# Performance work log

Hardware: AMD Instinct MI355X
Metric: run time of the kernel (lower is better)

The kernel has to match this reference:

```python
import jax, jax.numpy as jnp
import numpy as np

N_NODES = 100000
N_EDGES = 1600000
C_IN = 63
C_OUT = 63


def _glorot(key, shape):
    lim = (6.0 / (shape[0] + shape[1])) ** 0.5
    return jax.random.uniform(key, shape, jnp.float32, -lim, lim)


def setup_inputs() -> dict:
    key = jax.random.key(0)
    ks = jax.random.split(key, 10)
    t = jax.random.uniform(ks[0], (1,), jnp.float32)
    data = jax.random.normal(ks[1], (N_NODES, C_IN), jnp.float32)
    edges = jax.random.randint(ks[2], (2, N_EDGES), 0, N_NODES, jnp.int64)
    pos = jax.random.normal(ks[3], (N_NODES, 3), jnp.float32)
    edge_attr = jax.random.uniform(ks[4], (N_EDGES,), jnp.float32)
    # GCNConv(c_in+1, 64) -> GCNConv(64, 32) -> GCNConv(32, c_out)
    W1 = _glorot(ks[5], (C_IN + 1, 64)); b1 = jnp.zeros((64,), jnp.float32)
    W2 = _glorot(ks[6], (64, 32));       b2 = jnp.zeros((32,), jnp.float32)
    W3 = _glorot(ks[7], (32, C_OUT));    b3 = jnp.zeros((C_OUT,), jnp.float32)
    return {"t": t, "data": data, "edges": edges, "pos": pos,
            "edge_attr": edge_attr, "W1": W1, "b1": b1, "W2": W2,
            "b2": b2, "W3": W3, "b3": b3}


def _gcn_conv(x, W, b, row, col, norm, self_norm, n):
    # PyG GCNConv: linear, then normalized scatter-add aggregation (+self-loop), then bias
    x = x @ W                                                    # [N, F_out]
    out = jax.ops.segment_sum(x[row] * norm[:, None], col, num_segments=n)
    out = out + x * self_norm[:, None]                           # self-loop term
    return out + b


def reference(t, data, edges, pos, edge_attr, W1, b1, W2, b2, W3, b3):
    n = data.shape[0]
    row, col = edges[0], edges[1]                                # source j, target i
    ew = edge_attr.astype(jnp.float32)
    # gcn_norm with self-loops (fill_value=1): deg over target incl. self-loop
    deg = jax.ops.segment_sum(ew, col, num_segments=n) + 1.0
    dis = jnp.where(deg > 0, jax.lax.rsqrt(deg), 0.0)
    norm = dis[row] * ew * dis[col]                              # [E]
    self_norm = dis * dis                                        # [N]
    # time channel concat
    tt = jnp.ones((n, 1), data.dtype) * t
    h = jnp.concatenate([tt, data.astype(jnp.float32)], axis=1)  # [N, c_in+1]
    h = jnp.tanh(_gcn_conv(h, W1, b1, row, col, norm, self_norm, n))
    h = jnp.tanh(_gcn_conv(h, W2, b2, row, col, norm, self_norm, n))
    return _gcn_conv(h, W3, b3, row, col, norm, self_norm, n)
```

## Files before the change

kernel.cpp:

```cpp
#include <hip/hip_runtime.h>
#include <hip/hip_fp16.h>


static inline int cdiv64(long long a, int b) { return (int)((a + b - 1) / b); }

#define BSH 8
#define BCAP 8192
#define CHUNK 4096

typedef _Float16 half8v __attribute__((ext_vector_type(8)));
union F4H8 { float4 f4; half8v h; };

__device__ __forceinline__ float tanh_fast(float x) {
  float t = __expf(2.0f * x);
  float r = __builtin_amdgcn_rcpf(t + 1.0f);
  return fmaf(-2.0f, r, 1.0f);
}

__global__ void zero_kernel(int4* __restrict__ p, int n4) {
  int i = blockIdx.x * blockDim.x + threadIdx.x;
  if (i < n4) p[i] = make_int4(0, 0, 0, 0);
}

__global__ __launch_bounds__(256) void bucket1_kernel(
    const int* __restrict__ row, const int* __restrict__ col,
    const float* __restrict__ ew, int* __restrict__ gcur,
    uint2* __restrict__ btmp, int nE, int nb) {
  __shared__ int hcnt[512];
  __shared__ int gbase[512];
  const int tid = threadIdx.x;
  const int e0 = blockIdx.x * CHUNK;
  const int cnt_e = min(CHUNK, nE - e0);
  for (int i = tid; i < nb; i += 256) hcnt[i] = 0;
  __syncthreads();

  uint2 recs[CHUNK / 256];
  int   bs[CHUNK / 256];
  int   lis[CHUNK / 256];
#pragma unroll
  for (int p = 0; p < CHUNK / 256; ++p) {
    int k = tid + p * 256;
    bool valid = k < cnt_e;
    int e = e0 + (valid ? k : 0);
    int c = col[e];
    unsigned q = __float2uint_rn(ew[e] * 32768.0f);
    if (q > 32767u) q = 32767u;
    uint2 r;
    r.x = (q << 17) | (unsigned)row[e];
    r.y = (unsigned)c;
    int b = c >> BSH;
    recs[p] = r;
    bs[p] = valid ? b : -1;
    lis[p] = valid ? atomicAdd(&hcnt[b], 1) : 0;
  }
  __syncthreads();
  for (int i = tid; i < nb; i += 256)
    gbase[i] = hcnt[i] ? atomicAdd(&gcur[i], hcnt[i]) : 0;
  __syncthreads();
#pragma unroll
  for (int p = 0; p < CHUNK / 256; ++p) {
    int b = bs[p];
    if (b >= 0) {
      int idx = gbase[b] + lis[p];
      if (idx < BCAP) btmp[((size_t)b << 13) + idx] = recs[p];
    }
  }
}

__global__ __launch_bounds__(256) void bucket2_kernel(
    const int* __restrict__ gcur, const uint2* __restrict__ btmp,
    uint2* __restrict__ ce, int2* __restrict__ node2,
    float* __restrict__ dis, int n) {
  __shared__ uint2 recs[BCAP];
  __shared__ uint2 stageA[BCAP / 2];
  __shared__ uint2 stageB[BCAP / 2];
  __shared__ unsigned cnt[256], sumq[256], start[256], cur[256], scanbuf[256];
  const int tid = threadIdx.x;
  const int b = blockIdx.x;
  const int cb = min(gcur[b], BCAP);
  const int colbase = b << BSH;
  const int ncols = min(256, n - colbase);

  cnt[tid] = 0; sumq[tid] = 0; cur[tid] = 0;
  const uint2* src = btmp + ((size_t)b << 13);
  for (int k = tid; k < cb; k += 256) recs[k] = src[k];
  __syncthreads();
  for (int k = tid; k < cb; k += 256) {
    unsigned cl = recs[k].y & 255u;
    atomicAdd(&cnt[cl], 1u);
    atomicAdd(&sumq[cl], recs[k].x >> 17);
  }
  __syncthreads();
  unsigned v = cnt[tid];
  unsigned incl = v;
  scanbuf[tid] = incl;
  __syncthreads();
  for (int off = 1; off < 256; off <<= 1) {
    unsigned add = (tid >= off) ? scanbuf[tid - off] : 0u;
    __syncthreads();
    incl += add;
    scanbuf[tid] = incl;
    __syncthreads();
  }
  start[tid] = incl - v;
  __syncthreads();
  for (int k = tid; k < cb; k += 256) {
    unsigned rw = recs[k].x;
    unsigned cl = recs[k].y & 255u;
    unsigned p = start[cl] + atomicAdd(&cur[cl], 1u);
    uint2 o;
    o.x = rw & 0x1FFFFu;
    o.y = __float_as_uint((float)(rw >> 17) * 3.0517578125e-05f);
    if (p < (unsigned)(BCAP / 2)) stageA[p] = o;
    else stageB[p - BCAP / 2] = o;
  }
  __syncthreads();
  const unsigned base = (unsigned)b << 13;
  for (int k = tid; k < cb; k += 256)
    ce[base + k] = (k < BCAP / 2) ? stageA[k] : stageB[k - BCAP / 2];
  if (tid < ncols) {
    node2[colbase + tid] = make_int2((int)(base + start[tid]), (int)cnt[tid]);
    float deg = (float)sumq[tid] * 3.0517578125e-05f + 1.0f;
    dis[colbase + tid] = rsqrtf(deg);
  }
}

__global__ __launch_bounds__(256) void gemm1_tiled(const float* __restrict__ data,
                                                   const float* __restrict__ tptr,
                                                   const float* __restrict__ W,
                                                   const float* __restrict__ dis,
                                                   __half2* __restrict__ y, int n) {
  __shared__ float Ws[64 * 64];
  __shared__ float Ds[64 * 63];
  const int tid = threadIdx.x;
  {
    const float4* W4 = (const float4*)W;
    float4* Ws4 = (float4*)Ws;
#pragma unroll
    for (int p = 0; p < 4; ++p) Ws4[p * 256 + tid] = W4[p * 256 + tid];
  }
  const float tv = tptr[0];
  const int rbase = blockIdx.x * 64;
  const int limit = min(64, n - rbase) * 63;
  {
    const float4* s4 = (const float4*)(data + (size_t)rbase * 63);
    float4* d4 = (float4*)Ds;
    const int n4 = limit >> 2;
#pragma unroll
    for (int p = 0; p < 4; ++p) {
      int idx = p * 256 + tid;
      if (idx < n4) d4[idx] = s4[idx];
    }
    int tail = limit & 3;
    if (tid < tail) Ds[(n4 << 2) + tid] = data[(size_t)rbase * 63 + (n4 << 2) + tid];
  }
  __syncthreads();
  const int tx = tid & 15, ty = tid >> 4;
  const float* a0p = &Ds[(4 * ty + 0) * 63];
  const float* a1p = &Ds[(4 * ty + 1) * 63];
  const float* a2p = &Ds[(4 * ty + 2) * 63];
  const float* a3p = &Ds[(4 * ty + 3) * 63];
  float acc[4][4];
  {
    float4 w0 = *(const float4*)&Ws[4 * tx];
#pragma unroll
    for (int i = 0; i < 4; ++i) {
      acc[i][0] = tv * w0.x; acc[i][1] = tv * w0.y;
      acc[i][2] = tv * w0.z; acc[i][3] = tv * w0.w;
    }
  }
#pragma unroll 3
  for (int k = 0; k < 63; ++k) {
    float4 w4 = *(const float4*)&Ws[(k + 1) * 64 + 4 * tx];
    float a0 = a0p[k], a1 = a1p[k], a2 = a2p[k], a3 = a3p[k];
    acc[0][0] = fmaf(a0, w4.x, acc[0][0]); acc[0][1] = fmaf(a0, w4.y, acc[0][1]);
    acc[0][2] = fmaf(a0, w4.z, acc[0][2]); acc[0][3] = fmaf(a0, w4.w, acc[0][3]);
    acc[1][0] = fmaf(a1, w4.x, acc[1][0]); acc[1][1] = fmaf(a1, w4.y, acc[1][1]);
    acc[1][2] = fmaf(a1, w4.z, acc[1][2]); acc[1][3] = fmaf(a1, w4.w, acc[1][3]);
    acc[2][0] = fmaf(a2, w4.x, acc[2][0]); acc[2][1] = fmaf(a2, w4.y, acc[2][1]);
    acc[2][2] = fmaf(a2, w4.z, acc[2][2]); acc[2][3] = fmaf(a2, w4.w, acc[2][3]);
    acc[3][0] = fmaf(a3, w4.x, acc[3][0]); acc[3][1] = fmaf(a3, w4.y, acc[3][1]);
    acc[3][2] = fmaf(a3, w4.z, acc[3][2]); acc[3][3] = fmaf(a3, w4.w, acc[3][3]);
  }
#pragma unroll
  for (int i = 0; i < 4; ++i) {
    int r = rbase + 4 * ty + i;
    if (r < n) {
      float di = dis[r];
      __half2* yp = y + (long long)r * 32 + 2 * tx;
      yp[0] = __floats2half2_rn(acc[i][0] * di, acc[i][1] * di);
      yp[1] = __floats2half2_rn(acc[i][2] * di, acc[i][3] * di);
    }
  }
}

__global__ void gather64h(const __half2* __restrict__ x, const uint2* __restrict__ ce,
                          const int2* __restrict__ node2, const float* __restrict__ dis,
                          const float* __restrict__ b, __half2* __restrict__ o, int n) {
  int i = blockIdx.x * 4 + (threadIdx.x >> 6);
  if (i >= n) return;
  int lane = threadIdx.x & 63;
  int g = lane >> 3;
  int f8 = lane & 7;
  int2 sc = node2[i];
  const uint2* cb = ce + sc.x;
  int c = sc.y;
  const float4* xf = (const float4*)x;
  float4 accA = {0.f, 0.f, 0.f, 0.f}, accB = {0.f, 0.f, 0.f, 0.f};
  int k = g;
  uint2 rec = (k < c) ? cb[k] : make_uint2(0u, 0u);
  while (k < c) {
    int kn = k + 8;
    uint2 recn = (kn < c) ? cb[kn] : make_uint2(0u, 0u);
    float w = __uint_as_float(rec.y);
    F4H8 u; u.f4 = xf[(size_t)rec.x * 8 + f8];
    accA.x = fmaf((float)u.h[0], w, accA.x);
    accA.y = fmaf((float)u.h[1], w, accA.y);
    accA.z = fmaf((float)u.h[2], w, accA.z);
    accA.w = fmaf((float)u.h[3], w, accA.w);
    accB.x = fmaf((float)u.h[4], w, accB.x);
    accB.y = fmaf((float)u.h[5], w, accB.y);
    accB.z = fmaf((float)u.h[6], w, accB.z);
    accB.w = fmaf((float)u.h[7], w, accB.w);
    rec = recn; k = kn;
  }
#pragma unroll
  for (int d = 8; d <= 32; d <<= 1) {
    accA.x += __shfl_xor(accA.x, d, 64); accA.y += __shfl_xor(accA.y, d, 64);
    accA.z += __shfl_xor(accA.z, d, 64); accA.w += __shfl_xor(accA.w, d, 64);
    accB.x += __shfl_xor(accB.x, d, 64); accB.y += __shfl_xor(accB.y, d, 64);
    accB.z += __shfl_xor(accB.z, d, 64); accB.w += __shfl_xor(accB.w, d, 64);
  }
  if (g == 0) {
    F4H8 s; s.f4 = xf[(size_t)i * 8 + f8];
    float di = dis[i];
    float4 b0 = ((const float4*)b)[2 * f8];
    float4 b1 = ((const float4*)b)[2 * f8 + 1];
    float v0 = tanh_fast(di * (accA.x + (float)s.h[0]) + b0.x);
    float v1 = tanh_fast(di * (accA.y + (float)s.h[1]) + b0.y);
    float v2 = tanh_fast(di * (accA.z + (float)s.h[2]) + b0.z);
    float v3 = tanh_fast(di * (accA.w + (float)s.h[3]) + b0.w);
    float v4 = tanh_fast(di * (accB.x + (float)s.h[4]) + b1.x);
    float v5 = tanh_fast(di * (accB.y + (float)s.h[5]) + b1.y);
    float v6 = tanh_fast(di * (accB.z + (float)s.h[6]) + b1.z);
    float v7 = tanh_fast(di * (accB.w + (float)s.h[7]) + b1.w);
    __half2 r0 = __floats2half2_rn(v0, v1);
    __half2 r1 = __floats2half2_rn(v2, v3);
    __half2 r2 = __floats2half2_rn(v4, v5);
    __half2 r3 = __floats2half2_rn(v6, v7);
    float4 st;
    st.x = *reinterpret_cast<float*>(&r0);
    st.y = *reinterpret_cast<float*>(&r1);
    st.z = *reinterpret_cast<float*>(&r2);
    st.w = *reinterpret_cast<float*>(&r3);
    ((float4*)o)[(size_t)i * 8 + f8] = st;
  }
}

template <bool TANH, bool BIAS, bool POSTDIS, bool FOUT>
__global__ void gather32h(const __half2* __restrict__ x, const uint2* __restrict__ ce,
                          const int2* __restrict__ node2, const float* __restrict__ dis,
                          const float* __restrict__ b, void* __restrict__ outv, int n) {
  int i = blockIdx.x * 4 + (threadIdx.x >> 6);
  if (i >= n) return;
  int lane = threadIdx.x & 63;
  int g = lane >> 2;
  int f8 = lane & 3;
  int2 sc = node2[i];
  const uint2* cb = ce + sc.x;
  int c = sc.y;
  const float4* xf = (const float4*)x;
  float4 accA = {0.f, 0.f, 0.f, 0.f}, accB = {0.f, 0.f, 0.f, 0.f};
  int k = g;
  uint2 rec = (k < c) ? cb[k] : make_uint2(0u, 0u);
  while (k < c) {
    int kn = k + 16;
    uint2 recn = (kn < c) ? cb[kn] : make_uint2(0u, 0u);
    float w = __uint_as_float(rec.y);
    F4H8 u; u.f4 = xf[(size_t)rec.x * 4 + f8];
    accA.x = fmaf((float)u.h[0], w, accA.x);
    accA.y = fmaf((float)u.h[1], w, accA.y);
    accA.z = fmaf((float)u.h[2], w, accA.z);
    accA.w = fmaf((float)u.h[3], w, accA.w);
    accB.x = fmaf((float)u.h[4], w, accB.x);
    accB.y = fmaf((float)u.h[5], w, accB.y);
    accB.z = fmaf((float)u.h[6], w, accB.z);
    accB.w = fmaf((float)u.h[7], w, accB.w);
    rec = recn; k = kn;
  }
#pragma unroll
  for (int d = 4; d <= 32; d <<= 1) {
    accA.x += __shfl_xor(accA.x, d, 64); accA.y += __shfl_xor(accA.y, d, 64);
    accA.z += __shfl_xor(accA.z, d, 64); accA.w += __shfl_xor(accA.w, d, 64);
    accB.x += __shfl_xor(accB.x, d, 64); accB.y += __shfl_xor(accB.y, d, 64);
    accB.z += __shfl_xor(accB.z, d, 64); accB.w += __shfl_xor(accB.w, d, 64);
  }
  if (g == 0) {
    F4H8 s; s.f4 = xf[(size_t)i * 4 + f8];
    float di = dis[i];
    float v0 = di * (accA.x + (float)s.h[0]);
    float v1 = di * (accA.y + (float)s.h[1]);
    float v2 = di * (accA.z + (float)s.h[2]);
    float v3 = di * (accA.w + (float)s.h[3]);
    float v4 = di * (accB.x + (float)s.h[4]);
    float v5 = di * (accB.y + (float)s.h[5]);
    float v6 = di * (accB.z + (float)s.h[6]);
    float v7 = di * (accB.w + (float)s.h[7]);
    if (BIAS) {
      float4 b0 = ((const float4*)b)[2 * f8];
      float4 b1 = ((const float4*)b)[2 * f8 + 1];
      v0 += b0.x; v1 += b0.y; v2 += b0.z; v3 += b0.w;
      v4 += b1.x; v5 += b1.y; v6 += b1.z; v7 += b1.w;
    }
    if (TANH) {
      v0 = tanh_fast(v0); v1 = tanh_fast(v1); v2 = tanh_fast(v2); v3 = tanh_fast(v3);
      v4 = tanh_fast(v4); v5 = tanh_fast(v5); v6 = tanh_fast(v6); v7 = tanh_fast(v7);
    }
    if (POSTDIS) {
      v0 *= di; v1 *= di; v2 *= di; v3 *= di;
      v4 *= di; v5 *= di; v6 *= di; v7 *= di;
    }
    if (FOUT) {
      ((float4*)outv)[(size_t)i * 8 + 2 * f8]     = make_float4(v0, v1, v2, v3);
      ((float4*)outv)[(size_t)i * 8 + 2 * f8 + 1] = make_float4(v4, v5, v6, v7);
    } else {
      __half2 r0 = __floats2half2_rn(v0, v1);
      __half2 r1 = __floats2half2_rn(v2, v3);
      __half2 r2 = __floats2half2_rn(v4, v5);
      __half2 r3 = __floats2half2_rn(v6, v7);
      float4 st;
      st.x = *reinterpret_cast<float*>(&r0);
      st.y = *reinterpret_cast<float*>(&r1);
      st.z = *reinterpret_cast<float*>(&r2);
      st.w = *reinterpret_cast<float*>(&r3);
      ((float4*)outv)[(size_t)i * 4 + f8] = st;
    }
  }
}

__global__ __launch_bounds__(256) void gemm2t(const __half2* __restrict__ h1,
                                              const float* __restrict__ W,
                                              const float* __restrict__ dis,
                                              __half2* __restrict__ y2, int n) {
  __shared__ float As[64 * 65];
  __shared__ float Ws[64 * 32];
  const int tid = threadIdx.x;
  const int rbase = blockIdx.x * 64;
  const int rows = min(64, n - rbase);
  {
    const float4* W4 = (const float4*)W;
    float4* Ws4 = (float4*)Ws;
    Ws4[tid] = W4[tid];
    Ws4[256 + tid] = W4[256 + tid];
  }
  {
    const __half2* src = h1 + (size_t)rbase * 32;
    const int limit = rows * 32;
#pragma unroll
    for (int p = 0; p < 8; ++p) {
      int idx = p * 256 + tid;
      if (idx < limit) {
        float2 f = __half22float2(src[idx]);
        int r = idx >> 5, k2 = idx & 31;
        As[r * 65 + 2 * k2] = f.x;
        As[r * 65 + 2 * k2 + 1] = f.y;
      }
    }
  }
  __syncthreads();
  const int tx = tid & 7, ty = tid >> 3;
  const float* a0p = &As[(2 * ty) * 65];
  const float* a1p = &As[(2 * ty + 1) * 65];
  float acc0[4] = {0.f, 0.f, 0.f, 0.f};
  float acc1[4] = {0.f, 0.f, 0.f, 0.f};
#pragma unroll 4
  for (int k = 0; k < 64; ++k) {
    float4 w4 = *(const float4*)&Ws[k * 32 + 4 * tx];
    float a0 = a0p[k], a1 = a1p[k];
    acc0[0] = fmaf(a0, w4.x, acc0[0]); acc0[1] = fmaf(a0, w4.y, acc0[1]);
    acc0[2] = fmaf(a0, w4.z, acc0[2]); acc0[3] = fmaf(a0, w4.w, acc0[3]);
    acc1[0] = fmaf(a1, w4.x, acc1[0]); acc1[1] = fmaf(a1, w4.y, acc1[1]);
    acc1[2] = fmaf(a1, w4.z, acc1[2]); acc1[3] = fmaf(a1, w4.w, acc1[3]);
  }
  int r0 = rbase + 2 * ty, r1 = r0 + 1;
  if (r0 < n) {
    float di = dis[r0];
    __half2 h0 = __floats2half2_rn(acc0[0] * di, acc0[1] * di);
    __half2 h1v = __floats2half2_rn(acc0[2] * di, acc0[3] * di);
    float2 st;
    st.x = *reinterpret_cast<float*>(&h0);
    st.y = *reinterpret_cast<float*>(&h1v);
    ((float2*)y2)[(size_t)r0 * 8 + tx] = st;
  }
  if (r1 < n) {
    float di = dis[r1];
    __half2 h0 = __floats2half2_rn(acc1[0] * di, acc1[1] * di);
    __half2 h1v = __floats2half2_rn(acc1[2] * di, acc1[3] * di);
    float2 st;
    st.x = *reinterpret_cast<float*>(&h0);
    st.y = *reinterpret_cast<float*>(&h1v);
    ((float2*)y2)[(size_t)r1 * 8 + tx] = st;
  }
}

__global__ __launch_bounds__(256) void gemm3_tiled(const float* __restrict__ agg,
                                                   const float* __restrict__ W,
                                                   const float* __restrict__ b,
                                                   float* __restrict__ out, int n) {
  __shared__ float As[64 * 33];
  __shared__ float Ws[32 * 64];
  const int tid = threadIdx.x;
  const int rbase = blockIdx.x * 64;
  const int rows = min(64, n - rbase);
  {
    int r = tid >> 6, j = tid & 63;
#pragma unroll
    for (int p = 0; p < 8; ++p) {
      int rr = r + p * 4;
      if (j < 63) Ws[rr * 64 + j] = W[rr * 63 + j];
    }
    const float* src = agg + (size_t)rbase * 32;
    const int limit = rows * 32;
#pragma unroll
    for (int p = 0; p < 8; ++p) {
      int idx = p * 256 + tid;
      if (idx < limit) As[(idx >> 5) * 33 + (idx & 31)] = src[idx];
    }
  }
  __syncthreads();
  const int tx = tid & 15, ty = tid >> 4;
  const float* a0p = &As[(4 * ty + 0) * 33];
  const float* a1p = &As[(4 * ty + 1) * 33];
  const float* a2p = &As[(4 * ty + 2) * 33];
  const float* a3p = &As[(4 * ty + 3) * 33];
  float bb[4];
#pragma unroll
  for (int jj = 0; jj < 4; ++jj) {
    int j = 4 * tx + jj;
    bb[jj] = (j < 63) ? b[j] : 0.f;
  }
  float acc[4][4];
#pragma unroll
  for (int i = 0; i < 4; ++i) {
    acc[i][0] = bb[0]; acc[i][1] = bb[1]; acc[i][2] = bb[2]; acc[i][3] = bb[3];
  }
#pragma unroll
  for (int k = 0; k < 32; ++k) {
    float4 w4 = *(const float4*)&Ws[k * 64 + 4 * tx];
    float a0 = a0p[k], a1 = a1p[k], a2 = a2p[k], a3 = a3p[k];
    acc[0][0] = fmaf(a0, w4.x, acc[0][0]); acc[0][1] = fmaf(a0, w4.y, acc[0][1]);
    acc[0][2] = fmaf(a0, w4.z, acc[0][2]); acc[0][3] = fmaf(a0, w4.w, acc[0][3]);
    acc[1][0] = fmaf(a1, w4.x, acc[1][0]); acc[1][1] = fmaf(a1, w4.y, acc[1][1]);
    acc[1][2] = fmaf(a1, w4.z, acc[1][2]); acc[1][3] = fmaf(a1, w4.w, acc[1][3]);
    acc[2][0] = fmaf(a2, w4.x, acc[2][0]); acc[2][1] = fmaf(a2, w4.y, acc[2][1]);
    acc[2][2] = fmaf(a2, w4.z, acc[2][2]); acc[2][3] = fmaf(a2, w4.w, acc[2][3]);
    acc[3][0] = fmaf(a3, w4.x, acc[3][0]); acc[3][1] = fmaf(a3, w4.y, acc[3][1]);
    acc[3][2] = fmaf(a3, w4.z, acc[3][2]); acc[3][3] = fmaf(a3, w4.w, acc[3][3]);
  }
#pragma unroll
  for (int i = 0; i < 4; ++i) {
    int r = rbase + 4 * ty + i;
    if (r < n) {
      float* op = out + (size_t)r * 63 + 4 * tx;
#pragma unroll
      for (int jj = 0; jj < 4; ++jj)
        if (4 * tx + jj < 63) op[jj] = acc[i][jj];
    }
  }
}

extern "C" void kernel_launch(void* const* d_in, const int* in_sizes, int n_in,
                              void* d_out, int out_size, void* d_ws, size_t ws_size,
                              hipStream_t stream) {
  const float* t    = (const float*)d_in[0];
  const float* data = (const float*)d_in[1];
  const int*   edges = (const int*)d_in[2];
  const float* ew = (const float*)d_in[4];
  const float* W1 = (const float*)d_in[5];
  const float* b1 = (const float*)d_in[6];
  const float* W2 = (const float*)d_in[7];
  const float* b2 = (const float*)d_in[8];
  const float* W3 = (const float*)d_in[9];
  const float* b3 = (const float*)d_in[10];
  float* out = (float*)d_out;

  const int n  = in_sizes[1] / 63;
  const int nE = in_sizes[4];
  const int* row = edges;
  const int* col = edges + nE;
  const int nb = (n + 255) >> 8;

  float* ws    = (float*)d_ws;
  float* dis   = ws;
  int2*  node2 = (int2*)(ws + n);
  int*   gcur  = (int*)(ws + 3 * (size_t)n);
  uint2* ce    = (uint2*)(ws + 3 * (size_t)n + 512);
  size_t ceW   = (size_t)nb * BCAP;
  float* regA  = (float*)(ce + ceW);
  float* regB  = regA + (size_t)n * 32;
  uint2* btmp  = (uint2*)regA;

  const int B = 256;

  zero_kernel<<<1, 128, 0, stream>>>((int4*)gcur, 128);
  bucket1_kernel<<<cdiv64(nE, CHUNK), 256, 0, stream>>>(row, col, ew, gcur, btmp, nE, nb);
  bucket2_kernel<<<nb, 256, 0, stream>>>(gcur, btmp, ce, node2, dis, n);

  gemm1_tiled<<<cdiv64(n, 64), 256, 0, stream>>>(data, t, W1, dis, (__half2*)regA, n);
  gather64h<<<cdiv64(n, 4), B, 0, stream>>>((const __half2*)regA, ce, node2, dis, b1,
                                            (__half2*)regB, n);
  gemm2t<<<cdiv64(n, 64), 256, 0, stream>>>((const __half2*)regB, W2, dis, (__half2*)regA, n);
  gather32h<true, true, true, false><<<cdiv64(n, 4), B, 0, stream>>>(
      (const __half2*)regA, ce, node2, dis, b2, regB, n);
  gather32h<false, false, false, true><<<cdiv64(n, 4), B, 0, stream>>>(
      (const __half2*)regB, ce, node2, dis, nullptr, regA, n);
  gemm3_tiled<<<cdiv64(n, 64), 256, 0, stream>>>(regA, W3, b3, out, n);
}
```

Baseline: 244.9 us.

## Switch gather kernels to feature-per-lane scalar loads without shuffle reduction

Rewrites the 64- and 32-wide gather kernels so each lane owns one output feature and loops over all incident edges, loading a single fp16 value per edge. This removes the cross-lane shuffle reduction and the vectorized half8 unpacking. The 32-wide variant packs two nodes per wave. The trade-off is a longer serial edge loop per lane, narrower memory accesses and less independent load parallelism within a wave.

```diff
diff --git a/kernel.cpp b/kernel.cpp
--- a/kernel.cpp
+++ b/kernel.cpp
@@ -7,9 +7,6 @@
 #define BSH 8
 #define BCAP 8192
 #define CHUNK 4096
-
-typedef _Float16 half8v __attribute__((ext_vector_type(8)));
-union F4H8 { float4 f4; half8v h; };
 
 __device__ __forceinline__ float tanh_fast(float x) {
   float t = __expf(2.0f * x);
@@ -194,148 +191,59 @@
   }
 }
 
-__global__ void gather64h(const __half2* __restrict__ x, const uint2* __restrict__ ce,
+__global__ void gather64h(const _Float16* __restrict__ x, const uint2* __restrict__ ce,
                           const int2* __restrict__ node2, const float* __restrict__ dis,
-                          const float* __restrict__ b, __half2* __restrict__ o, int n) {
+                          const float* __restrict__ b, _Float16* __restrict__ o, int n) {
   int i = blockIdx.x * 4 + (threadIdx.x >> 6);
   if (i >= n) return;
-  int lane = threadIdx.x & 63;
-  int g = lane >> 3;
-  int f8 = lane & 7;
+  unsigned lane = threadIdx.x & 63u;
   int2 sc = node2[i];
   const uint2* cb = ce + sc.x;
   int c = sc.y;
-  const float4* xf = (const float4*)x;
-  float4 accA = {0.f, 0.f, 0.f, 0.f}, accB = {0.f, 0.f, 0.f, 0.f};
-  int k = g;
-  uint2 rec = (k < c) ? cb[k] : make_uint2(0u, 0u);
-  while (k < c) {
-    int kn = k + 8;
-    uint2 recn = (kn < c) ? cb[kn] : make_uint2(0u, 0u);
+  float acc = 0.f;
+  uint2 rec = (c > 0) ? cb[0] : make_uint2(0u, 0u);
+  for (int k = 0; k < c; ++k) {
+    uint2 recn = (k + 1 < c) ? cb[k + 1] : make_uint2(0u, 0u);
     float w = __uint_as_float(rec.y);
-    F4H8 u; u.f4 = xf[(size_t)rec.x * 8 + f8];
-    accA.x = fmaf((float)u.h[0], w, accA.x);
-    accA.y = fmaf((float)u.h[1], w, accA.y);
-    accA.z = fmaf((float)u.h[2], w, accA.z);
-    accA.w = fmaf((float)u.h[3], w, accA.w);
-    accB.x = fmaf((float)u.h[4], w, accB.x);
-    accB.y = fmaf((float)u.h[5], w, accB.y);
-    accB.z = fmaf((float)u.h[6], w, accB.z);
-    accB.w = fmaf((float)u.h[7], w, accB.w);
-    rec = recn; k = kn;
-  }
-#pragma unroll
-  for (int d = 8; d <= 32; d <<= 1) {
-    accA.x += __shfl_xor(accA.x, d, 64); accA.y += __shfl_xor(accA.y, d, 64);
-    accA.z += __shfl_xor(accA.z, d, 64); accA.w += __shfl_xor(accA.w, d, 64);
-    accB.x += __shfl_xor(accB.x, d, 64); accB.y += __shfl_xor(accB.y, d, 64);
-    accB.z += __shfl_xor(accB.z, d, 64); accB.w += __shfl_xor(accB.w, d, 64);
-  }
-  if (g == 0) {
-    F4H8 s; s.f4 = xf[(size_t)i * 8 + f8];
-    float di = dis[i];
-    float4 b0 = ((const float4*)b)[2 * f8];
-    float4 b1 = ((const float4*)b)[2 * f8 + 1];
-    float v0 = tanh_fast(di * (accA.x + (float)s.h[0]) + b0.x);
-    float v1 = tanh_fast(di * (accA.y + (float)s.h[1]) + b0.y);
-    float v2 = tanh_fast(di * (accA.z + (float)s.h[2]) + b0.z);
-    float v3 = tanh_fast(di * (accA.w + (float)s.h[3]) + b0.w);
-    float v4 = tanh_fast(di * (accB.x + (float)s.h[4]) + b1.x);
-    float v5 = tanh_fast(di * (accB.y + (float)s.h[5]) + b1.y);
-    float v6 = tanh_fast(di * (accB.z + (float)s.h[6]) + b1.z);
-    float v7 = tanh_fast(di * (accB.w + (float)s.h[7]) + b1.w);
-    __half2 r0 = __floats2half2_rn(v0, v1);
-    __half2 r1 = __floats2half2_rn(v2, v3);
-    __half2 r2 = __floats2half2_rn(v4, v5);
-    __half2 r3 = __floats2half2_rn(v6, v7);
-    float4 st;
-    st.x = *reinterpret_cast<float*>(&r0);
-    st.y = *reinterpret_cast<float*>(&r1);
-    st.z = *reinterpret_cast<float*>(&r2);
-    st.w = *reinterpret_cast<float*>(&r3);
-    ((float4*)o)[(size_t)i * 8 + f8] = st;
-  }
+    float hv = (float)x[rec.x * 64u + lane];
+    acc = fmaf(hv, w, acc);
+    rec = recn;
+  }
+  float di = dis[i];
+  float self = (float)x[(unsigned)i * 64u + lane];
+  float v = tanh_fast(di * (acc + self) + b[lane]);
+  o[(unsigned)i * 64u + lane] = (_Float16)v;
 }
 
 template <bool TANH, bool BIAS, bool POSTDIS, bool FOUT>
-__global__ void gather32h(const __half2* __restrict__ x, const uint2* __restrict__ ce,
+__global__ void gather32h(const _Float16* __restrict__ x, const uint2* __restrict__ ce,
                           const int2* __restrict__ node2, const float* __restrict__ dis,
                           const float* __restrict__ b, void* __restrict__ outv, int n) {
-  int i = blockIdx.x * 4 + (threadIdx.x >> 6);
+  int lane = threadIdx.x & 63;
+  int half_id = lane >> 5;
+  unsigned f = (unsigned)(lane & 31);
+  int i = blockIdx.x * 8 + ((threadIdx.x >> 6) << 1) + half_id;
   if (i >= n) return;
-  int lane = threadIdx.x & 63;
-  int g = lane >> 2;
-  int f8 = lane & 3;
   int2 sc = node2[i];
   const uint2* cb = ce + sc.x;
   int c = sc.y;
-  const float4* xf = (const float4*)x;
-  float4 accA = {0.f, 0.f, 0.f, 0.f}, accB = {0.f, 0.f, 0.f, 0.f};
-  int k = g;
-  uint2 rec = (k < c) ? cb[k] : make_uint2(0u, 0u);
-  while (k < c) {
-    int kn = k + 16;
-    uint2 recn = (kn < c) ? cb[kn] : make_uint2(0u, 0u);
+  float acc = 0.f;
+  uint2 rec = (c > 0) ? cb[0] : make_uint2(0u, 0u);
+  for (int k = 0; k < c; ++k) {
+    uint2 recn = (k + 1 < c) ? cb[k + 1] : make_uint2(0u, 0u);
     float w = __uint_as_float(rec.y);
-    F4H8 u; u.f4 = xf[(size_t)rec.x * 4 + f8];
-    accA.x = fmaf((float)u.h[0], w, accA.x);
-    accA.y = fmaf((float)u.h[1], w, accA.y);
-    accA.z = fmaf((float)u.h[2], w, accA.z);
-    accA.w = fmaf((float)u.h[3], w, accA.w);
-    accB.x = fmaf((float)u.h[4], w, accB.x);
-    accB.y = fmaf((float)u.h[5], w, accB.y);
-    accB.z = fmaf((float)u.h[6], w, accB.z);
-    accB.w = fmaf((float)u.h[7], w, accB.w);
-    rec = recn; k = kn;
-  }
-#pragma unroll
-  for (int d = 4; d <= 32; d <<= 1) {
-    accA.x += __shfl_xor(accA.x, d, 64); accA.y += __shfl_xor(accA.y, d, 64);
-    accA.z += __shfl_xor(accA.z, d, 64); accA.w += __shfl_xor(accA.w, d, 64);
-    accB.x += __shfl_xor(accB.x, d, 64); accB.y += __shfl_xor(accB.y, d, 64);
-    accB.z += __shfl_xor(accB.z, d, 64); accB.w += __shfl_xor(accB.w, d, 64);
-  }
-  if (g == 0) {
-    F4H8 s; s.f4 = xf[(size_t)i * 4 + f8];
-    float di = dis[i];
-    float v0 = di * (accA.x + (float)s.h[0]);
-    float v1 = di * (accA.y + (float)s.h[1]);
-    float v2 = di * (accA.z + (float)s.h[2]);
-    float v3 = di * (accA.w + (float)s.h[3]);
-    float v4 = di * (accB.x + (float)s.h[4]);
-    float v5 = di * (accB.y + (float)s.h[5]);
-    float v6 = di * (accB.z + (float)s.h[6]);
-    float v7 = di * (accB.w + (float)s.h[7]);
-    if (BIAS) {
-      float4 b0 = ((const float4*)b)[2 * f8];
-      float4 b1 = ((const float4*)b)[2 * f8 + 1];
-      v0 += b0.x; v1 += b0.y; v2 += b0.z; v3 += b0.w;
-      v4 += b1.x; v5 += b1.y; v6 += b1.z; v7 += b1.w;
-    }
-    if (TANH) {
-      v0 = tanh_fast(v0); v1 = tanh_fast(v1); v2 = tanh_fast(v2); v3 = tanh_fast(v3);
-      v4 = tanh_fast(v4); v5 = tanh_fast(v5); v6 = tanh_fast(v6); v7 = tanh_fast(v7);
-    }
-    if (POSTDIS) {
-      v0 *= di; v1 *= di; v2 *= di; v3 *= di;
-      v4 *= di; v5 *= di; v6 *= di; v7 *= di;
-    }
-    if (FOUT) {
-      ((float4*)outv)[(size_t)i * 8 + 2 * f8]     = make_float4(v0, v1, v2, v3);
-      ((float4*)outv)[(size_t)i * 8 + 2 * f8 + 1] = make_float4(v4, v5, v6, v7);
-    } else {
-      __half2 r0 = __floats2half2_rn(v0, v1);
-      __half2 r1 = __floats2half2_rn(v2, v3);
-      __half2 r2 = __floats2half2_rn(v4, v5);
-      __half2 r3 = __floats2half2_rn(v6, v7);
-      float4 st;
-      st.x = *reinterpret_cast<float*>(&r0);
-      st.y = *reinterpret_cast<float*>(&r1);
-      st.z = *reinterpret_cast<float*>(&r2);
-      st.w = *reinterpret_cast<float*>(&r3);
-      ((float4*)outv)[(size_t)i * 4 + f8] = st;
-    }
-  }
+    float hv = (float)x[rec.x * 32u + f];
+    acc = fmaf(hv, w, acc);
+    rec = recn;
+  }
+  float di = dis[i];
+  float self = (float)x[(unsigned)i * 32u + f];
+  float v = di * (acc + self);
+  if (BIAS) v += b[f];
+  if (TANH) v = tanh_fast(v);
+  if (POSTDIS) v *= di;
+  if (FOUT) ((float*)outv)[(size_t)i * 32 + f] = v;
+  else ((_Float16*)outv)[(unsigned)i * 32u + f] = (_Float16)v;
 }
 
 __global__ __launch_bounds__(256) void gemm2t(const __half2* __restrict__ h1,
@@ -507,12 +415,12 @@
   bucket2_kernel<<<nb, 256, 0, stream>>>(gcur, btmp, ce, node2, dis, n);
 
   gemm1_tiled<<<cdiv64(n, 64), 256, 0, stream>>>(data, t, W1, dis, (__half2*)regA, n);
-  gather64h<<<cdiv64(n, 4), B, 0, stream>>>((const __half2*)regA, ce, node2, dis, b1,
-                                            (__half2*)regB, n);
+  gather64h<<<cdiv64(n, 4), B, 0, stream>>>((const _Float16*)regA, ce, node2, dis, b1,
+                                            (_Float16*)regB, n);
   gemm2t<<<cdiv64(n, 64), 256, 0, stream>>>((const __half2*)regB, W2, dis, (__half2*)regA, n);
-  gather32h<true, true, true, false><<<cdiv64(n, 4), B, 0, stream>>>(
-      (const __half2*)regA, ce, node2, dis, b2, regB, n);
-  gather32h<false, false, false, true><<<cdiv64(n, 4), B, 0, stream>>>(
-      (const __half2*)regB, ce, node2, dis, nullptr, regA, n);
+  gather32h<true, true, true, false><<<cdiv64(n, 8), B, 0, stream>>>(
+      (const _Float16*)regA, ce, node2, dis, b2, regB, n);
+  gather32h<false, false, false, true><<<cdiv64(n, 8), B, 0, stream>>>(
+      (const _Float16*)regB, ce, node2, dis, nullptr, regA, n);
   gemm3_tiled<<<cdiv64(n, 64), 256, 0, stream>>>(regA, W3, b3, out, n);
 }
```

Result: slower. 440.3 us (+79.8%).
